# Performance work log

Measured on AMD Instinct MI355X. Metric: run time of the kernel, lower is better.

## Reference

```python
import jax, jax.numpy as jnp
import numpy as np

C = 256; HEADS = 8; LEVELS = 4; POINTS = 4; D = C // HEADS
SPATIAL = np.array([[96, 96], [48, 48], [24, 24], [12, 12]], dtype=np.int32)  # (H, W) per level
AREAS = SPATIAL[:, 0] * SPATIAL[:, 1]
HW = int(AREAS.sum())  # 12240
LSI = np.concatenate([[0], np.cumsum(AREAS)[:-1]]).astype(np.int32)
N = 1; Q = HW


def setup_inputs() -> dict:
    key = jax.random.key(0)
    ks = jax.random.split(key, 12)
    s = 0.02
    return {
        "query": jax.random.normal(ks[0], (N, Q, C), jnp.float32),
        "reference_points": jax.random.uniform(ks[1], (N, Q, LEVELS, 2), jnp.float32),
        "input_flatten": jax.random.normal(ks[2], (N, HW, C), jnp.float32),
        "input_spatial_shapes": jnp.asarray(SPATIAL),
        "input_level_start_index": jnp.asarray(LSI),
        "W_off": jax.random.normal(ks[3], (C, HEADS * LEVELS * POINTS * 2), jnp.float32) * s,
        "b_off": jax.random.normal(ks[4], (HEADS * LEVELS * POINTS * 2,), jnp.float32) * s,
        "W_attn": jax.random.normal(ks[5], (C, HEADS * LEVELS * POINTS), jnp.float32) * s,
        "b_attn": jax.random.normal(ks[6], (HEADS * LEVELS * POINTS,), jnp.float32) * s,
        "W_val": jax.random.normal(ks[7], (C, C), jnp.float32) * (1.0 / np.sqrt(C)),
        "b_val": jax.random.normal(ks[8], (C,), jnp.float32) * s,
        "W_out": jax.random.normal(ks[9], (C, C), jnp.float32) * (1.0 / np.sqrt(C)),
        "b_out": jax.random.normal(ks[10], (C,), jnp.float32) * s,
    }


def _ms_deform_attn(query, reference_points, input_flatten, sp, lsi,
                    W_off, b_off, W_attn, b_attn, W_val, b_val, W_out, b_out):
    n, q, c = query.shape
    hw = input_flatten.shape[1]
    # value projection -> [N, Hd, HW, D]
    value = (input_flatten @ W_val + b_val).reshape(n, hw, HEADS, D).transpose(0, 2, 1, 3)
    # sampling offsets [N,Q,Hd,L,P,2]
    off = (query @ W_off + b_off).reshape(n, q, HEADS, LEVELS, POINTS, 2)
    # attention weights softmaxed over L*P (done inside the fused CUDA kernel)
    attn = jax.nn.softmax((query @ W_attn + b_attn).reshape(n, q, HEADS, LEVELS * POINTS), axis=-1)
    attn = attn.reshape(n, q, HEADS, LEVELS, POINTS)
    # normalized sampling locations (reference_points last dim == 2 branch)
    norm = jnp.stack([sp[:, 1], sp[:, 0]], -1).astype(query.dtype)  # (W, H) per level
    loc = reference_points[:, :, None, :, None, :] + off / norm[None, None, None, :, None, :]
    Hl = sp[:, 0][None, None, None, :, None]
    Wl = sp[:, 1][None, None, None, :, None]
    start = lsi[None, None, None, :, None]
    # grid_sample-style (align_corners=False) pixel coordinates
    x = loc[..., 0] * Wl - 0.5
    y = loc[..., 1] * Hl - 0.5
    x0 = jnp.floor(x); y0 = jnp.floor(y)
    lx = x - x0; ly = y - y0
    x0i = x0.astype(jnp.int32); y0i = y0.astype(jnp.int32)

    def gather(yi, xi):
        valid = (xi >= 0) & (xi < Wl) & (yi >= 0) & (yi < Hl)
        idx = jnp.where(valid, start + yi * Wl + xi, 0)  # [N,Q,Hd,L,P]
        idx_t = idx.transpose(0, 2, 1, 3, 4).reshape(n, HEADS, q * LEVELS * POINTS, 1)
        g = jnp.take_along_axis(value, idx_t, axis=2)  # [N,Hd,Q*L*P,D]
        g = g.reshape(n, HEADS, q, LEVELS, POINTS, D)
        return g * valid.transpose(0, 2, 1, 3, 4)[..., None]

    def w(a):
        return a.transpose(0, 2, 1, 3, 4)[..., None]  # [N,Hd,Q,L,P,1]

    sampled = (gather(y0i, x0i) * w((1 - ly) * (1 - lx))
               + gather(y0i, x0i + 1) * w((1 - ly) * lx)
               + gather(y0i + 1, x0i) * w(ly * (1 - lx))
               + gather(y0i + 1, x0i + 1) * w(ly * lx))  # [N,Hd,Q,L,P,D]
    out = jnp.einsum('nhqlpd,nqhlp->nqhd', sampled, attn).reshape(n, q, c)
    return out @ W_out + b_out


def reference(query, reference_points, input_flatten, input_spatial_shapes, input_level_start_index,
              W_off, b_off, W_attn, b_attn, W_val, b_val, W_out, b_out):
    return _ms_deform_attn(query, reference_points, input_flatten,
                           input_spatial_shapes, input_level_start_index,
                           W_off, b_off, W_attn, b_attn, W_val, b_val, W_out, b_out)
```

## Files before the change

### kernel.cpp

```cpp
#include <hip/hip_runtime.h>

#define QTOT 12240
#define KD   256

typedef float f32x4 __attribute__((ext_vector_type(4)));
typedef short s16x8 __attribute__((ext_vector_type(8)));
typedef short s16x4 __attribute__((ext_vector_type(4)));
typedef unsigned short ushort_t;

__device__ __forceinline__ unsigned short f2b(float x) {
    union { float f; unsigned u; } c; c.f = x;
    unsigned r = c.u + 0x7fffu + ((c.u >> 16) & 1u);
    return (unsigned short)(r >> 16);
}
__device__ __forceinline__ float b2f(unsigned short u) {
    return __uint_as_float((unsigned)u << 16);
}
__device__ __forceinline__ int swz(int row, int kb) { return row * 512 + (kb ^ ((row & 7) << 4)); }

__global__ __launch_bounds__(256) void prep(
    const float* __restrict__ W_val, const float* __restrict__ W_off,
    const float* __restrict__ W_attn, const float* __restrict__ W_out,
    const float* __restrict__ b_off, const float* __restrict__ b_attn,
    ushort_t* __restrict__ WvT, ushort_t* __restrict__ WcT,
    ushort_t* __restrict__ WoT, float* __restrict__ bcomb)
{
    int id = blockIdx.x * 256 + threadIdx.x;
    if (id < 65536) { int n = id >> 8, k = id & 255; WvT[id] = f2b(W_val[k * 256 + n]); }
    else if (id < 163840) {
        int t = id - 65536; int n = t >> 8, k = t & 255;
        float v = (n < 256) ? W_off[k * 256 + n] : W_attn[k * 128 + (n - 256)];
        WcT[t] = f2b(v);
    } else if (id < 229376) {
        int t = id - 163840; int n = t >> 8, k = t & 255;
        WoT[t] = f2b(W_out[k * 256 + n]);
    } else if (id < 229760) {
        int t = id - 229376; bcomb[t] = (t < 256) ? b_off[t] : b_attn[t - 256];
    }
}

__global__ __launch_bounds__(256) void gemm1(
    const float* __restrict__ inflat, const float* __restrict__ query,
    const ushort_t* __restrict__ WvT, const ushort_t* __restrict__ WcT,
    const float* __restrict__ b_val, const float* __restrict__ bcomb,
    ushort_t* __restrict__ projb, ushort_t* __restrict__ offb,
    ushort_t* __restrict__ attnb)
{
    __shared__ char As[16384];
    const int b = blockIdx.x;
    const bool isval = b < 383;
    const int bm = (isval ? b : b - 383) * 32;
    const float* A = isval ? inflat : query;
    const ushort_t* WT = isval ? WvT : WcT;
    const int nc = isval ? 4 : 6;

    const int tid = threadIdx.x, lane = tid & 63, wave = tid >> 6;
    const int lr = lane & 15, g8 = (lane >> 4) * 8;

    {
        const float4* srcb = (const float4*)(A + (size_t)bm * KD);
        const int rem_rows = QTOT - bm;
#pragma unroll
        for (int j = 0; j < 8; ++j) {
            const int f4i = j * 256 + tid;
            const int row = f4i >> 6;
            const int colb = (f4i & 63) * 8;
            float4 f = make_float4(0.f, 0.f, 0.f, 0.f);
            if (row < rem_rows) f = srcb[f4i];
            s16x4 v;
            v[0] = f2b(f.x); v[1] = f2b(f.y); v[2] = f2b(f.z); v[3] = f2b(f.w);
            *(s16x4*)(As + swz(row, colb)) = v;
        }
    }
    __syncthreads();

    const int rg = (lane >> 4) * 4;

    for (int c = 0; c < nc; ++c) {
        const int col = c * 64 + wave * 16 + lr;
        s16x8 bfr[8];
        {
            const ushort_t* bp = WT + (size_t)col * KD + g8;
#pragma unroll
            for (int kc = 0; kc < 8; ++kc) bfr[kc] = *(const s16x8*)(bp + kc * 32);
        }
        f32x4 acc[2];
        acc[0] = (f32x4)0.f; acc[1] = (f32x4)0.f;
#pragma unroll
        for (int kc = 0; kc < 8; ++kc) {
            const int kb = (kc * 32 + g8) * 2;
            s16x8 a0 = *(const s16x8*)(As + swz(lr,      kb));
            s16x8 a1 = *(const s16x8*)(As + swz(16 + lr, kb));
            acc[0] = __builtin_amdgcn_mfma_f32_16x16x32_bf16(a0, bfr[kc], acc[0], 0, 0, 0);
            acc[1] = __builtin_amdgcn_mfma_f32_16x16x32_bf16(a1, bfr[kc], acc[1], 0, 0, 0);
        }
        const float bb = isval ? b_val[col] : bcomb[col];

        if (!isval && c >= 4) {
            const int gh = (c - 4) * 4 + wave;
            float v[2][4], m[2][4], e[2][4], s[2][4];
#pragma unroll
            for (int mf = 0; mf < 2; ++mf)
#pragma unroll
                for (int rr = 0; rr < 4; ++rr) { v[mf][rr] = acc[mf][rr] + bb; m[mf][rr] = v[mf][rr]; }
#pragma unroll
            for (int d = 1; d < 16; d <<= 1)
#pragma unroll
                for (int mf = 0; mf < 2; ++mf)
#pragma unroll
                    for (int rr = 0; rr < 4; ++rr) m[mf][rr] = fmaxf(m[mf][rr], __shfl_xor(m[mf][rr], d));
#pragma unroll
            for (int mf = 0; mf < 2; ++mf)
#pragma unroll
                for (int rr = 0; rr < 4; ++rr) { e[mf][rr] = __expf(v[mf][rr] - m[mf][rr]); s[mf][rr] = e[mf][rr]; }
#pragma unroll
            for (int d = 1; d < 16; d <<= 1)
#pragma unroll
                for (int mf = 0; mf < 2; ++mf)
#pragma unroll
                    for (int rr = 0; rr < 4; ++rr) s[mf][rr] += __shfl_xor(s[mf][rr], d);
#pragma unroll
            for (int mf = 0; mf < 2; ++mf)
#pragma unroll
                for (int rr = 0; rr < 4; ++rr) {
                    const int row = bm + mf * 16 + rg + rr;
                    if (row < QTOT)
                        attnb[(size_t)row * 128 + gh * 16 + lr] = f2b(e[mf][rr] / s[mf][rr]);
                }
        } else {
#pragma unroll
            for (int mf = 0; mf < 2; ++mf)
#pragma unroll
                for (int rr = 0; rr < 4; ++rr) {
                    const int row = bm + mf * 16 + rg + rr;
                    if (row >= QTOT) continue;
                    const float v = acc[mf][rr] + bb;
                    if (isval) projb[(size_t)row * 256 + col] = f2b(v);
                    else       offb [(size_t)row * 256 + col] = f2b(v);
                }
        }
    }
}

__global__ __launch_bounds__(256) void sample6(
    const float* __restrict__ rp, const ushort_t* __restrict__ offb,
    const ushort_t* __restrict__ attnb, const ushort_t* __restrict__ projb,
    const int* __restrict__ sp, const int* __restrict__ lsi,
    ushort_t* __restrict__ outpre)
{
    const int bid = blockIdx.x;
    const int hh = (bid >= 1530) ? 1 : 0;
    const int g  = hh ? (bid - 1530) : bid;
    const int q0 = g * 8;
    const int tid = threadIdx.x;

    __shared__ int   s_idx[512][4];
    __shared__ float s_w[512][4];

#pragma unroll
    for (int rep = 0; rep < 2; ++rep) {
        const int task = rep * 256 + tid;
        const int ql = task >> 6;
        const int hp = (task >> 4) & 3;
        const int lp = task & 15;
        const int l = lp >> 2;
        const int q = q0 + ql;
        const int gh = hh * 4 + hp;
        const int t128 = gh * 16 + lp;

        const float aw = b2f(attnb[(size_t)q * 128 + t128]);

        const unsigned opk = *(const unsigned*)&offb[(size_t)q * 256 + t128 * 2];
        const float ox = __uint_as_float(opk << 16);
        const float oy = __uint_as_float(opk & 0xffff0000u);

        const int Hl = sp[l * 2], Wl = sp[l * 2 + 1], st = lsi[l];
        const float rx = rp[((size_t)q * 4 + l) * 2 + 0];
        const float ry = rp[((size_t)q * 4 + l) * 2 + 1];

        const float x = rx * (float)Wl + ox - 0.5f;
        const float y = ry * (float)Hl + oy - 0.5f;
        const float xf = floorf(x), yf = floorf(y);
        const int x0 = (int)xf, y0 = (int)yf;
        const float lx = x - xf, ly = y - yf;

        const bool vx0 = (x0 >= 0) && (x0 < Wl);
        const bool vx1 = (x0 + 1 >= 0) && (x0 + 1 < Wl);
        const bool vy0 = (y0 >= 0) && (y0 < Hl);
        const bool vy1 = (y0 + 1 >= 0) && (y0 + 1 < Hl);

        s_w[task][0] = (vx0 && vy0) ? aw * (1.f - ly) * (1.f - lx) : 0.f;
        s_w[task][1] = (vx1 && vy0) ? aw * (1.f - ly) * lx         : 0.f;
        s_w[task][2] = (vx0 && vy1) ? aw * ly * (1.f - lx)         : 0.f;
        s_w[task][3] = (vx1 && vy1) ? aw * ly * lx                 : 0.f;
        s_idx[task][0] = (vx0 && vy0) ? (st + y0 * Wl + x0) * 512           : 0;
        s_idx[task][1] = (vx1 && vy0) ? (st + y0 * Wl + x0 + 1) * 512       : 0;
        s_idx[task][2] = (vx0 && vy1) ? (st + (y0 + 1) * Wl + x0) * 512     : 0;
        s_idx[task][3] = (vx1 && vy1) ? (st + (y0 + 1) * Wl + x0 + 1) * 512 : 0;
    }
    __syncthreads();

    const int c8 = tid & 3;
    const int pq = (tid >> 2) & 1;
    const int hp = (tid >> 3) & 3;
    const int ql = tid >> 5;
    const int gh = hh * 4 + hp;
    const char* basec = (const char*)projb + (gh * 32 + c8 * 8) * 2;
    const int slot0 = (ql << 6) | (hp << 4);

    float a0 = 0, a1 = 0, a2 = 0, a3 = 0, a4 = 0, a5 = 0, a6 = 0, a7 = 0;
#pragma unroll
    for (int l = 0; l < 4; ++l) {
#pragma unroll
        for (int j = 0; j < 2; ++j) {
            const int slot = slot0 | (l << 2) | (pq * 2 + j);
            const int4   i4 = *(const int4*)s_idx[slot];
            const float4 w4 = *(const float4*)s_w[slot];
#pragma unroll
            for (int c = 0; c < 4; ++c) {
                const int   id = (c == 0) ? i4.x : (c == 1) ? i4.y : (c == 2) ? i4.z : i4.w;
                const float w  = (c == 0) ? w4.x : (c == 1) ? w4.y : (c == 2) ? w4.z : w4.w;
                const uint4 v = *(const uint4*)(basec + id);
                a0 += w * __uint_as_float(v.x << 16);
                a1 += w * __uint_as_float(v.x & 0xffff0000u);
                a2 += w * __uint_as_float(v.y << 16);
                a3 += w * __uint_as_float(v.y & 0xffff0000u);
                a4 += w * __uint_as_float(v.z << 16);
                a5 += w * __uint_as_float(v.z & 0xffff0000u);
                a6 += w * __uint_as_float(v.w << 16);
                a7 += w * __uint_as_float(v.w & 0xffff0000u);
            }
        }
    }
    a0 += __shfl_xor(a0, 4); a1 += __shfl_xor(a1, 4);
    a2 += __shfl_xor(a2, 4); a3 += __shfl_xor(a3, 4);
    a4 += __shfl_xor(a4, 4); a5 += __shfl_xor(a5, 4);
    a6 += __shfl_xor(a6, 4); a7 += __shfl_xor(a7, 4);

    if (pq == 0) {
        uint4 o;
        o.x = (unsigned)f2b(a0) | ((unsigned)f2b(a1) << 16);
        o.y = (unsigned)f2b(a2) | ((unsigned)f2b(a3) << 16);
        o.z = (unsigned)f2b(a4) | ((unsigned)f2b(a5) << 16);
        o.w = (unsigned)f2b(a6) | ((unsigned)f2b(a7) << 16);
        *(uint4*)&outpre[(size_t)(q0 + ql) * 256 + gh * 32 + c8 * 8] = o;
    }
}

__global__ __launch_bounds__(256) void gemm_o(
    const ushort_t* __restrict__ Ab, const ushort_t* __restrict__ WoT,
    const float* __restrict__ b_out, float* __restrict__ out)
{
    const int bm = blockIdx.x * 32;
    const int tid = threadIdx.x, lane = tid & 63, wave = tid >> 6;
    const int lr = lane & 15, g8 = (lane >> 4) * 8;
    const int rg = (lane >> 4) * 4;

    const ushort_t* ap0;
    const ushort_t* ap1;
    {
        int r0 = bm + lr;      if (r0 >= QTOT) r0 = QTOT - 1;
        int r1 = bm + 16 + lr; if (r1 >= QTOT) r1 = QTOT - 1;
        ap0 = Ab + (size_t)r0 * KD + g8;
        ap1 = Ab + (size_t)r1 * KD + g8;
    }

#pragma unroll
    for (int c = 0; c < 4; ++c) {
        const int col = c * 64 + wave * 16 + lr;
        s16x8 bfr[8];
        {
            const ushort_t* bp = WoT + (size_t)col * KD + g8;
#pragma unroll
            for (int kc = 0; kc < 8; ++kc) bfr[kc] = *(const s16x8*)(bp + kc * 32);
        }
        f32x4 acc[2];
        acc[0] = (f32x4)0.f; acc[1] = (f32x4)0.f;
#pragma unroll
        for (int kc = 0; kc < 8; ++kc) {
            s16x8 a0 = *(const s16x8*)(ap0 + kc * 32);
            s16x8 a1 = *(const s16x8*)(ap1 + kc * 32);
            acc[0] = __builtin_amdgcn_mfma_f32_16x16x32_bf16(a0, bfr[kc], acc[0], 0, 0, 0);
            acc[1] = __builtin_amdgcn_mfma_f32_16x16x32_bf16(a1, bfr[kc], acc[1], 0, 0, 0);
        }
        const float bb = b_out[col];
#pragma unroll
        for (int mf = 0; mf < 2; ++mf)
#pragma unroll
            for (int rr = 0; rr < 4; ++rr) {
                const int row = bm + mf * 16 + rg + rr;
                if (row < QTOT) out[(size_t)row * 256 + col] = acc[mf][rr] + bb;
            }
    }
}

extern "C" void kernel_launch(void* const* d_in, const int* in_sizes, int n_in,
                              void* d_out, int out_size, void* d_ws, size_t ws_size,
                              hipStream_t stream) {
    const float* query  = (const float*)d_in[0];
    const float* rp     = (const float*)d_in[1];
    const float* inflat = (const float*)d_in[2];
    const int*   sp     = (const int*)d_in[3];
    const int*   lsi    = (const int*)d_in[4];
    const float* W_off  = (const float*)d_in[5];
    const float* b_off  = (const float*)d_in[6];
    const float* W_attn = (const float*)d_in[7];
    const float* b_attn = (const float*)d_in[8];
    const float* W_val  = (const float*)d_in[9];
    const float* b_val  = (const float*)d_in[10];
    const float* W_out  = (const float*)d_in[11];
    const float* b_out  = (const float*)d_in[12];
    float* out = (float*)d_out;

    char* ws = (char*)d_ws;
    ushort_t* projb  = (ushort_t*)ws; ws += (size_t)QTOT * 256 * 2;
    ushort_t* offb   = (ushort_t*)ws; ws += (size_t)QTOT * 256 * 2;
    ushort_t* attnb  = (ushort_t*)ws; ws += (size_t)QTOT * 128 * 2;
    ushort_t* outpre = (ushort_t*)ws; ws += (size_t)QTOT * 256 * 2;
    ushort_t* WvT    = (ushort_t*)ws; ws += 65536 * 2;
    ushort_t* WcT    = (ushort_t*)ws; ws += 98304 * 2;
    ushort_t* WoT    = (ushort_t*)ws; ws += 65536 * 2;
    float*    bcomb  = (float*)ws;    ws += 384 * 4;

    prep<<<dim3(898), dim3(256), 0, stream>>>(W_val, W_off, W_attn, W_out, b_off, b_attn,
                                              WvT, WcT, WoT, bcomb);

    gemm1<<<dim3(766), dim3(256), 0, stream>>>(inflat, query, WvT, WcT, b_val, bcomb,
                                               projb, offb, attnb);

    sample6<<<dim3(3060), dim3(256), 0, stream>>>(rp, offb, attnb, projb, sp, lsi, outpre);

    gemm_o<<<dim3(383), dim3(256), 0, stream>>>(outpre, WoT, b_out, out);
}
```

Baseline: 67.03 us.

## Fuse deformable sampling with output projection GEMM in one kernel

Merges the bilinear sampling kernel and the output projection GEMM into a single kernel. Each block samples 8 queries across all 8 heads into a swizzled shared buffer and then applies W_out via MFMA. This removes the intermediate bf16 buffer round trip and one launch. It also hardcodes square level shapes and packs index and bf16 weight into one int per corner to halve shared metadata. In exchange, each block reloads the full W_out from cache for only 8 rows, and half of each 16-row MFMA tile is unused.

```diff
diff --git a/kernel.cpp b/kernel.cpp
--- a/kernel.cpp
+++ b/kernel.cpp
@@ -142,31 +142,24 @@
     }
 }
 
-__global__ __launch_bounds__(256) void sample6(
+__global__ __launch_bounds__(256) void sample_proj(
     const float* __restrict__ rp, const ushort_t* __restrict__ offb,
     const ushort_t* __restrict__ attnb, const ushort_t* __restrict__ projb,
-    const int* __restrict__ sp, const int* __restrict__ lsi,
-    ushort_t* __restrict__ outpre)
+    const ushort_t* __restrict__ WoT, const float* __restrict__ b_out,
+    float* __restrict__ out)
 {
-    const int bid = blockIdx.x;
-    const int hh = (bid >= 1530) ? 1 : 0;
-    const int g  = hh ? (bid - 1530) : bid;
-    const int q0 = g * 8;
+    __shared__ int4 s_meta[1024];
+    __shared__ char outp[8192];
+
+    const int q0 = blockIdx.x * 8;
     const int tid = threadIdx.x;
 
-    __shared__ int   s_idx[512][4];
-    __shared__ float s_w[512][4];
-
-#pragma unroll
-    for (int rep = 0; rep < 2; ++rep) {
+#pragma unroll
+    for (int rep = 0; rep < 4; ++rep) {
         const int task = rep * 256 + tid;
-        const int ql = task >> 6;
-        const int hp = (task >> 4) & 3;
-        const int lp = task & 15;
-        const int l = lp >> 2;
+        const int ql = task >> 7, t128 = task & 127;
+        const int l = (t128 >> 2) & 3;
         const int q = q0 + ql;
-        const int gh = hh * 4 + hp;
-        const int t128 = gh * 16 + lp;
 
         const float aw = b2f(attnb[(size_t)q * 128 + t128]);
 
@@ -174,53 +167,57 @@
         const float ox = __uint_as_float(opk << 16);
         const float oy = __uint_as_float(opk & 0xffff0000u);
 
-        const int Hl = sp[l * 2], Wl = sp[l * 2 + 1], st = lsi[l];
+        const int Wl = 96 >> l;
+        const int st = 12288 - (12288 >> (2 * l));
         const float rx = rp[((size_t)q * 4 + l) * 2 + 0];
         const float ry = rp[((size_t)q * 4 + l) * 2 + 1];
 
         const float x = rx * (float)Wl + ox - 0.5f;
-        const float y = ry * (float)Hl + oy - 0.5f;
+        const float y = ry * (float)Wl + oy - 0.5f;
         const float xf = floorf(x), yf = floorf(y);
         const int x0 = (int)xf, y0 = (int)yf;
         const float lx = x - xf, ly = y - yf;
 
         const bool vx0 = (x0 >= 0) && (x0 < Wl);
         const bool vx1 = (x0 + 1 >= 0) && (x0 + 1 < Wl);
-        const bool vy0 = (y0 >= 0) && (y0 < Hl);
-        const bool vy1 = (y0 + 1 >= 0) && (y0 + 1 < Hl);
-
-        s_w[task][0] = (vx0 && vy0) ? aw * (1.f - ly) * (1.f - lx) : 0.f;
-        s_w[task][1] = (vx1 && vy0) ? aw * (1.f - ly) * lx         : 0.f;
-        s_w[task][2] = (vx0 && vy1) ? aw * ly * (1.f - lx)         : 0.f;
-        s_w[task][3] = (vx1 && vy1) ? aw * ly * lx                 : 0.f;
-        s_idx[task][0] = (vx0 && vy0) ? (st + y0 * Wl + x0) * 512           : 0;
-        s_idx[task][1] = (vx1 && vy0) ? (st + y0 * Wl + x0 + 1) * 512       : 0;
-        s_idx[task][2] = (vx0 && vy1) ? (st + (y0 + 1) * Wl + x0) * 512     : 0;
-        s_idx[task][3] = (vx1 && vy1) ? (st + (y0 + 1) * Wl + x0 + 1) * 512 : 0;
+        const bool vy0 = (y0 >= 0) && (y0 < Wl);
+        const bool vy1 = (y0 + 1 >= 0) && (y0 + 1 < Wl);
+
+        const float w00 = (vx0 && vy0) ? aw * (1.f - ly) * (1.f - lx) : 0.f;
+        const float w01 = (vx1 && vy0) ? aw * (1.f - ly) * lx         : 0.f;
+        const float w10 = (vx0 && vy1) ? aw * ly * (1.f - lx)         : 0.f;
+        const float w11 = (vx1 && vy1) ? aw * ly * lx                 : 0.f;
+        const int i00 = (vx0 && vy0) ? st + y0 * Wl + x0           : 0;
+        const int i01 = (vx1 && vy0) ? st + y0 * Wl + x0 + 1       : 0;
+        const int i10 = (vx0 && vy1) ? st + (y0 + 1) * Wl + x0     : 0;
+        const int i11 = (vx1 && vy1) ? st + (y0 + 1) * Wl + x0 + 1 : 0;
+
+        int4 m;
+        m.x = (i00 << 16) | (int)f2b(w00);
+        m.y = (i01 << 16) | (int)f2b(w01);
+        m.z = (i10 << 16) | (int)f2b(w10);
+        m.w = (i11 << 16) | (int)f2b(w11);
+        s_meta[task] = m;
     }
     __syncthreads();
 
-    const int c8 = tid & 3;
-    const int pq = (tid >> 2) & 1;
-    const int hp = (tid >> 3) & 3;
-    const int ql = tid >> 5;
-    const int gh = hh * 4 + hp;
-    const char* basec = (const char*)projb + (gh * 32 + c8 * 8) * 2;
-    const int slot0 = (ql << 6) | (hp << 4);
-
-    float a0 = 0, a1 = 0, a2 = 0, a3 = 0, a4 = 0, a5 = 0, a6 = 0, a7 = 0;
-#pragma unroll
-    for (int l = 0; l < 4; ++l) {
-#pragma unroll
-        for (int j = 0; j < 2; ++j) {
-            const int slot = slot0 | (l << 2) | (pq * 2 + j);
-            const int4   i4 = *(const int4*)s_idx[slot];
-            const float4 w4 = *(const float4*)s_w[slot];
+    {
+        const int c8 = tid & 3;
+        const int h = (tid >> 2) & 7;
+        const int ql = tid >> 5;
+        const char* basec = (const char*)projb + (h * 32 + c8 * 8) * 2;
+        const int slot0 = ql * 128 + h * 16;
+
+        float a0 = 0, a1 = 0, a2 = 0, a3 = 0, a4 = 0, a5 = 0, a6 = 0, a7 = 0;
+#pragma unroll
+        for (int lp = 0; lp < 16; ++lp) {
+            const int4 m = s_meta[slot0 + lp];
 #pragma unroll
             for (int c = 0; c < 4; ++c) {
-                const int   id = (c == 0) ? i4.x : (c == 1) ? i4.y : (c == 2) ? i4.z : i4.w;
-                const float w  = (c == 0) ? w4.x : (c == 1) ? w4.y : (c == 2) ? w4.z : w4.w;
-                const uint4 v = *(const uint4*)(basec + id);
+                const int pk = (c == 0) ? m.x : (c == 1) ? m.y : (c == 2) ? m.z : m.w;
+                const int off = (pk >> 16) << 9;
+                const float w = __uint_as_float((unsigned)pk << 16);
+                const uint4 v = *(const uint4*)(basec + off);
                 a0 += w * __uint_as_float(v.x << 16);
                 a1 += w * __uint_as_float(v.x & 0xffff0000u);
                 a2 += w * __uint_as_float(v.y << 16);
@@ -231,66 +228,42 @@
                 a7 += w * __uint_as_float(v.w & 0xffff0000u);
             }
         }
-    }
-    a0 += __shfl_xor(a0, 4); a1 += __shfl_xor(a1, 4);
-    a2 += __shfl_xor(a2, 4); a3 += __shfl_xor(a3, 4);
-    a4 += __shfl_xor(a4, 4); a5 += __shfl_xor(a5, 4);
-    a6 += __shfl_xor(a6, 4); a7 += __shfl_xor(a7, 4);
-
-    if (pq == 0) {
         uint4 o;
         o.x = (unsigned)f2b(a0) | ((unsigned)f2b(a1) << 16);
         o.y = (unsigned)f2b(a2) | ((unsigned)f2b(a3) << 16);
         o.z = (unsigned)f2b(a4) | ((unsigned)f2b(a5) << 16);
         o.w = (unsigned)f2b(a6) | ((unsigned)f2b(a7) << 16);
-        *(uint4*)&outpre[(size_t)(q0 + ql) * 256 + gh * 32 + c8 * 8] = o;
-    }
-}
-
-__global__ __launch_bounds__(256) void gemm_o(
-    const ushort_t* __restrict__ Ab, const ushort_t* __restrict__ WoT,
-    const float* __restrict__ b_out, float* __restrict__ out)
-{
-    const int bm = blockIdx.x * 32;
-    const int tid = threadIdx.x, lane = tid & 63, wave = tid >> 6;
-    const int lr = lane & 15, g8 = (lane >> 4) * 8;
-    const int rg = (lane >> 4) * 4;
-
-    const ushort_t* ap0;
-    const ushort_t* ap1;
+        *(uint4*)(outp + swz(ql, (h * 32 + c8 * 8) * 2)) = o;
+    }
+    __syncthreads();
+
     {
-        int r0 = bm + lr;      if (r0 >= QTOT) r0 = QTOT - 1;
-        int r1 = bm + 16 + lr; if (r1 >= QTOT) r1 = QTOT - 1;
-        ap0 = Ab + (size_t)r0 * KD + g8;
-        ap1 = Ab + (size_t)r1 * KD + g8;
-    }
-
-#pragma unroll
-    for (int c = 0; c < 4; ++c) {
-        const int col = c * 64 + wave * 16 + lr;
-        s16x8 bfr[8];
-        {
-            const ushort_t* bp = WoT + (size_t)col * KD + g8;
-#pragma unroll
-            for (int kc = 0; kc < 8; ++kc) bfr[kc] = *(const s16x8*)(bp + kc * 32);
-        }
-        f32x4 acc[2];
-        acc[0] = (f32x4)0.f; acc[1] = (f32x4)0.f;
-#pragma unroll
-        for (int kc = 0; kc < 8; ++kc) {
-            s16x8 a0 = *(const s16x8*)(ap0 + kc * 32);
-            s16x8 a1 = *(const s16x8*)(ap1 + kc * 32);
-            acc[0] = __builtin_amdgcn_mfma_f32_16x16x32_bf16(a0, bfr[kc], acc[0], 0, 0, 0);
-            acc[1] = __builtin_amdgcn_mfma_f32_16x16x32_bf16(a1, bfr[kc], acc[1], 0, 0, 0);
-        }
-        const float bb = b_out[col];
-#pragma unroll
-        for (int mf = 0; mf < 2; ++mf)
+        const int lane = tid & 63, wave = tid >> 6;
+        const int lr = lane & 15, g8 = (lane >> 4) * 8, rg = (lane >> 4) * 4;
+
+#pragma unroll
+        for (int nf = 0; nf < 4; ++nf) {
+            const int col = wave * 64 + nf * 16 + lr;
+            s16x8 bfr[8];
+            {
+                const ushort_t* bp = WoT + (size_t)col * KD + g8;
+#pragma unroll
+                for (int kc = 0; kc < 8; ++kc) bfr[kc] = *(const s16x8*)(bp + kc * 32);
+            }
+            f32x4 acc = (f32x4)0.f;
+#pragma unroll
+            for (int kc = 0; kc < 8; ++kc) {
+                s16x8 af = *(const s16x8*)(outp + swz(lr, (kc * 32 + g8) * 2));
+                acc = __builtin_amdgcn_mfma_f32_16x16x32_bf16(af, bfr[kc], acc, 0, 0, 0);
+            }
+            const float bb = b_out[col];
 #pragma unroll
             for (int rr = 0; rr < 4; ++rr) {
-                const int row = bm + mf * 16 + rg + rr;
-                if (row < QTOT) out[(size_t)row * 256 + col] = acc[mf][rr] + bb;
+                const int row = rg + rr;
+                if (row < 8)
+                    out[(size_t)(q0 + row) * 256 + col] = acc[rr] + bb;
             }
+        }
     }
 }
 
@@ -300,8 +273,6 @@
     const float* query  = (const float*)d_in[0];
     const float* rp     = (const float*)d_in[1];
     const float* inflat = (const float*)d_in[2];
-    const int*   sp     = (const int*)d_in[3];
-    const int*   lsi    = (const int*)d_in[4];
     const float* W_off  = (const float*)d_in[5];
     const float* b_off  = (const float*)d_in[6];
     const float* W_attn = (const float*)d_in[7];
@@ -316,7 +287,6 @@
     ushort_t* projb  = (ushort_t*)ws; ws += (size_t)QTOT * 256 * 2;
     ushort_t* offb   = (ushort_t*)ws; ws += (size_t)QTOT * 256 * 2;
     ushort_t* attnb  = (ushort_t*)ws; ws += (size_t)QTOT * 128 * 2;
-    ushort_t* outpre = (ushort_t*)ws; ws += (size_t)QTOT * 256 * 2;
     ushort_t* WvT    = (ushort_t*)ws; ws += 65536 * 2;
     ushort_t* WcT    = (ushort_t*)ws; ws += 98304 * 2;
     ushort_t* WoT    = (ushort_t*)ws; ws += 65536 * 2;
@@ -328,7 +298,6 @@
     gemm1<<<dim3(766), dim3(256), 0, stream>>>(inflat, query, WvT, WcT, b_val, bcomb,
                                                projb, offb, attnb);
 
-    sample6<<<dim3(3060), dim3(256), 0, stream>>>(rp, offb, attnb, projb, sp, lsi, outpre);
-
-    gemm_o<<<dim3(383), dim3(256), 0, stream>>>(outpre, WoT, b_out, out);
-}
+    sample_proj<<<dim3(1530), dim3(256), 0, stream>>>(rp, offb, attnb, projb,
+                                                      WoT, b_out, out);
+}
```

Result: slower. 82.56 us (+23.2%).
